# Kernel tuning notes

Measured on AMD Instinct MI355X. Metric: run time of the kernel, lower is better.

## Reference

```python
import jax, jax.numpy as jnp
import numpy as np

B, S, D, H = 2, 2048, 1024, 16
DK = D // H


def setup_inputs() -> dict:
    key = jax.random.key(0)
    ks = jax.random.split(key, 12)
    q = jax.random.normal(ks[0], (B, S, D), dtype=jnp.float32)
    k = jax.random.normal(ks[1], (B, S, D), dtype=jnp.float32)
    v = jax.random.normal(ks[2], (B, S, D), dtype=jnp.float32)
    # causal mask: 1 = attend, 0 = masked (masked_fill(mask==0, -inf))
    mask = jnp.tril(jnp.ones((S, S), dtype=jnp.int32))[None, None]
    w = 0.02
    Wq = jax.random.normal(ks[3], (D, D), dtype=jnp.float32) * w
    bq = jnp.zeros((D,), dtype=jnp.float32)
    Wk = jax.random.normal(ks[4], (D, D), dtype=jnp.float32) * w
    bk = jnp.zeros((D,), dtype=jnp.float32)
    Wv = jax.random.normal(ks[5], (D, D), dtype=jnp.float32) * w
    bv = jnp.zeros((D,), dtype=jnp.float32)
    Wo = jax.random.normal(ks[6], (D, D), dtype=jnp.float32) * w
    bo = jnp.zeros((D,), dtype=jnp.float32)
    return {"q": q, "k": k, "v": v, "mask": mask,
            "Wq": Wq, "bq": bq, "Wk": Wk, "bk": bk,
            "Wv": Wv, "bv": bv, "Wo": Wo, "bo": bo}


def _split_heads(x):
    b, s, _ = x.shape
    return x.reshape(b, s, H, DK).transpose(0, 2, 1, 3)  # [B,H,S,DK]


def reference(q, k, v, mask, Wq, bq, Wk, bk, Wv, bv, Wo, bo):
    qh = _split_heads(q @ Wq.T + bq)
    kh = _split_heads(k @ Wk.T + bk)
    vh = _split_heads(v @ Wv.T + bv)
    scale = 1.0 / jnp.sqrt(jnp.float32(DK))
    scores = jnp.einsum("bhqd,bhkd->bhqk", qh, kh) * scale  # [B,H,S,S]
    scores = jnp.where(mask == 0, -jnp.inf, scores)
    pesos = jax.nn.softmax(scores, axis=-1)
    pesos = jnp.nan_to_num(pesos, nan=0.0)  # fully-masked rows -> 0
    out = jnp.einsum("bhqk,bhkd->bhqd", pesos, vh)
    out = out.transpose(0, 2, 1, 3).reshape(q.shape[0], q.shape[1], D)
    # dropout is identity at inference
    return out @ Wo.T + bo
```

## Files before the change

### kernel.cpp

```cpp
#include <hip/hip_runtime.h>
#include <hip/hip_bf16.h>

#define B_  2
#define S_  2048
#define D_  1024
#define H_  16
#define DK_ 64

using bf16 = __hip_bfloat16;
typedef __bf16 bf16x8 __attribute__((ext_vector_type(8)));
typedef float  f32x4  __attribute__((ext_vector_type(4)));
typedef float  f32x16 __attribute__((ext_vector_type(16)));

__device__ inline void st1(float* p, float v) { *p = v; }
__device__ inline void st1(bf16*  p, float v) { *p = __float2bfloat16(v); }

__device__ inline void gll16(const bf16* g, bf16* l) {
    __builtin_amdgcn_global_load_lds(
        (const __attribute__((address_space(1))) unsigned int*)g,
        (__attribute__((address_space(3))) unsigned int*)l, 16, 0, 0);
}

__device__ inline f32x16 mfma32(bf16x8 a, bf16x8 b, f32x16 c) {
    return __builtin_amdgcn_mfma_f32_32x32x16_bf16(a, b, c, 0, 0, 0);
}

__device__ inline unsigned cvtpk(float lo, float hi) {
    unsigned r;
    asm("v_cvt_pk_bf16_f32 %0, %1, %2" : "=v"(r) : "v"(lo), "v"(hi));
    return r;
}

__device__ inline void plswap(unsigned &d, unsigned &s) {
    asm volatile("v_permlane32_swap_b32 %0, %1" : "+v"(d), "+v"(s));
}

__global__ __launch_bounds__(256) void cvt_kernel(
    const float* __restrict__ s0, const float* __restrict__ s1,
    const float* __restrict__ s2, const float* __restrict__ s3,
    const float* __restrict__ s4, const float* __restrict__ s5,
    const float* __restrict__ s6,
    bf16* __restrict__ d0, bf16* __restrict__ d1, bf16* __restrict__ d2,
    bf16* __restrict__ d3, bf16* __restrict__ d4, bf16* __restrict__ d5,
    bf16* __restrict__ d6, int nbig, int nsmall)
{
    const int z = blockIdx.y;
    const float* s; bf16* d; int n;
    switch (z) {
        case 0: s = s0; d = d0; n = nbig;   break;
        case 1: s = s1; d = d1; n = nbig;   break;
        case 2: s = s2; d = d2; n = nbig;   break;
        case 3: s = s3; d = d3; n = nsmall; break;
        case 4: s = s4; d = d4; n = nsmall; break;
        case 5: s = s5; d = d5; n = nsmall; break;
        default: s = s6; d = d6; n = nsmall; break;
    }
    const int idx = (blockIdx.x * 256 + threadIdx.x) * 4;
    if (idx < n) {
        const float4 v = *reinterpret_cast<const float4*>(s + idx);
        union { ushort4 u; __bf16 h[4]; } r;
        r.h[0] = (__bf16)v.x; r.h[1] = (__bf16)v.y;
        r.h[2] = (__bf16)v.z; r.h[3] = (__bf16)v.w;
        *reinterpret_cast<ushort4*>(d + idx) = r.u;
    }
}

template <typename TC, bool VT3, int BM>
__global__ __launch_bounds__(256, BM == 128 ? 3 : 4) void gemm_bt_kernel(
    const bf16* __restrict__ A0, const bf16* __restrict__ A1, const bf16* __restrict__ A2,
    const bf16* __restrict__ W0, const bf16* __restrict__ W1, const bf16* __restrict__ W2,
    const float* __restrict__ b0, const float* __restrict__ b1, const float* __restrict__ b2,
    TC* __restrict__ C0, TC* __restrict__ C1, TC* __restrict__ C2,
    int M, int N, int K)
{
    const int z = blockIdx.z;
    const bf16*  A    = (z == 0) ? A0 : (z == 1) ? A1 : A2;
    const bf16*  W    = (z == 0) ? W0 : (z == 1) ? W1 : W2;
    const float* bias = (z == 0) ? b0 : (z == 1) ? b1 : b2;
    TC*          C    = (z == 0) ? C0 : (z == 1) ? C1 : C2;

    __shared__ bf16 As[BM][32];
    __shared__ bf16 Bs[128][32];

    const int t    = threadIdx.x;
    const int lane = t & 63;
    const int wave = t >> 6;
    const int quad = lane >> 4;
    const int l16  = lane & 15;
    const int wm   = wave >> 1;
    const int wn   = wave & 1;

    const int m0 = blockIdx.y * BM;
    const int n0 = blockIdx.x * 128;

    constexpr int RPW = BM / 4;
    constexpr int MI  = BM / 32;
    const int ar0 = wave * RPW + (lane >> 2);
    const int br0 = wave * 32  + (lane >> 2);
    const int c0  = (lane & 3) * 8;
    const bf16* Ab = A + (size_t)(m0 + ar0) * K + c0;
    const bf16* Bb = W + (size_t)(n0 + br0) * K + c0;
    bf16* asd = &As[wave * RPW][0];
    bf16* bsd = &Bs[wave * 32][0];

    f32x4 acc[MI][4] = {};

    for (int kt = 0; kt < K; kt += 32) {
        __syncthreads();
        gll16(Ab + kt, asd);
        if constexpr (BM == 128) gll16(Ab + 16 * K + kt, asd + 16 * 32);
        gll16(Bb + kt, bsd);
        gll16(Bb + 16 * K + kt, bsd + 16 * 32);
        __syncthreads();

        bf16x8 af[MI], bfr[4];
#pragma unroll
        for (int mi = 0; mi < MI; mi++)
            af[mi] = *reinterpret_cast<const bf16x8*>(&As[wm * (BM / 2) + mi * 16 + l16][quad * 8]);
#pragma unroll
        for (int ni = 0; ni < 4; ni++)
            bfr[ni] = *reinterpret_cast<const bf16x8*>(&Bs[wn * 64 + ni * 16 + l16][quad * 8]);
#pragma unroll
        for (int mi = 0; mi < MI; mi++)
#pragma unroll
            for (int ni = 0; ni < 4; ni++)
                acc[mi][ni] = __builtin_amdgcn_mfma_f32_16x16x32_bf16(
                    af[mi], bfr[ni], acc[mi][ni], 0, 0, 0);
    }

    if (VT3 && z == 2) {
#pragma unroll
        for (int ni = 0; ni < 4; ni++) {
            const int col = n0 + wn * 64 + ni * 16 + l16;
            const float bvv = bias[col];
            const int hh = col >> 6, dh = col & 63;
#pragma unroll
            for (int mi = 0; mi < MI; mi++) {
                const int rb  = m0 + wm * (BM / 2) + mi * 16 + quad * 4;
                const int bb  = rb >> 11;
                const int tok = rb & (S_ - 1);
                union { ushort4 u; __bf16 h[4]; } pk;
#pragma unroll
                for (int i = 0; i < 4; i++)
                    pk.h[i] = (__bf16)(acc[mi][ni][i] + bvv);
                bf16* vt = (bf16*)C + ((size_t)(bb * H_ + hh) * DK_ + dh) * S_ + tok;
                *reinterpret_cast<ushort4*>(vt) = pk.u;
            }
        }
    } else {
#pragma unroll
        for (int ni = 0; ni < 4; ni++) {
            const int col = n0 + wn * 64 + ni * 16 + l16;
            const float bvv = bias[col];
#pragma unroll
            for (int mi = 0; mi < MI; mi++) {
#pragma unroll
                for (int i = 0; i < 4; i++) {
                    const int row = m0 + wm * (BM / 2) + mi * 16 + quad * 4 + i;
                    st1(&C[(size_t)row * N + col], acc[mi][ni][i] + bvv);
                }
            }
        }
    }
}

__global__ __launch_bounds__(256, 1) void attn_kernel(
    const bf16* __restrict__ Qp, const bf16* __restrict__ Kp,
    const bf16* __restrict__ VT, bf16* __restrict__ AO)
{
    const int t    = threadIdx.x;
    const int lane = t & 63;
    const int wave = t >> 6;
    const int r31  = lane & 31;
    const int hl   = lane >> 5;
    const int l7   = lane & 7;

    const int pairi = blockIdx.x;
    const int TL    = 15 - pairi;
    const int TS    = pairi;
    const int h = blockIdx.y;
    const int b = blockIdx.z;
    const size_t bh = (size_t)b * S_ * D_ + (size_t)h * DK_;
    const bf16* vtb = VT + (size_t)(b * H_ + h) * DK_ * S_;

    __shared__ bf16 Ks[4][64][64];
    __shared__ bf16 Vs[4][64][64];

    const int sR  = lane >> 3;
    const int scg = ((lane & 7) ^ sR) * 8;

    const float QSC = 0.18033688f;
    const float NEG = -1e30f;

    bf16x8 ONES;
#pragma unroll
    for (int j = 0; j < 8; j++) ONES[j] = (__bf16)1.0f;

    const int nA   = 2 * TL + 2;
    const int ntot = 34;

    int til = TL;
    bf16x8 qf[4];
    {
        const bf16* qr = Qp + bh + (size_t)(TL * 128 + wave * 32 + r31) * D_ + 8 * hl;
#pragma unroll
        for (int d = 0; d < 4; d++) {
            qf[d] = *reinterpret_cast<const bf16x8*>(qr + 16 * d);
#pragma unroll
            for (int j = 0; j < 8; j++) qf[d][j] = (__bf16)((float)qf[d][j] * QSC);
        }
    }

    f32x16 oacc0 = {}, oacc1 = {}, lacc = {};

    auto stage = [&](int slot) {
        const int k0n = ((slot < nA) ? slot : slot - nA) * 64;
        const int bb  = slot & 3;
#pragma unroll
        for (int j = 0; j < 2; j++) {
            const int rb = wave * 16 + j * 8;
            gll16(Kp + bh + (size_t)(k0n + rb + sR) * D_ + scg, &Ks[bb][rb][0]);
            gll16(vtb + (size_t)(rb + sR) * S_ + k0n + scg,     &Vs[bb][rb][0]);
        }
    };

    stage(0);
    stage(1);

    int kcbase = 0;
    for (int it = 0; it < ntot; it++) {
        if (it + 2 < ntot) {
            stage(it + 2);
            asm volatile("s_waitcnt vmcnt(8)" ::: "memory");
        } else if (it + 1 < ntot) {
            asm volatile("s_waitcnt vmcnt(4)" ::: "memory");
        } else {
            asm volatile("s_waitcnt vmcnt(0)" ::: "memory");
        }
        __builtin_amdgcn_s_barrier();

        if (it == nA) {
            const int qb0 = til * 128 + wave * 32;
#pragma unroll
            for (int r = 0; r < 16; r++) {
                const int q = qb0 + (r & 3) + 8 * (r >> 2) + 4 * hl;
                const float inv = 1.0f / lacc[r];
                AO[bh + (size_t)q * D_ + r31]      = __float2bfloat16(oacc0[r] * inv);
                AO[bh + (size_t)q * D_ + 32 + r31] = __float2bfloat16(oacc1[r] * inv);
            }
            til = TS; kcbase = nA;
            const bf16* qr = Qp + bh + (size_t)(TS * 128 + wave * 32 + r31) * D_ + 8 * hl;
#pragma unroll
            for (int d = 0; d < 4; d++) {
                qf[d] = *reinterpret_cast<const bf16x8*>(qr + 16 * d);
#pragma unroll
                for (int j = 0; j < 8; j++) qf[d][j] = (__bf16)((float)qf[d][j] * QSC);
            }
            oacc0 = f32x16{}; oacc1 = f32x16{}; lacc = f32x16{};
        }

        const int kc  = it - kcbase;
        const int k0  = kc * 64;
        const int buf = it & 3;
        const int qw0 = til * 128 + wave * 32;

        if (k0 <= qw0 + 31) {
            f32x16 s0 = {}, s1 = {};
#pragma unroll
            for (int d = 0; d < 4; d++) {
                const int g = ((2 * d + hl) ^ l7) * 8;
                const bf16x8 kf0 = *reinterpret_cast<const bf16x8*>(&Ks[buf][r31][g]);
                const bf16x8 kf1 = *reinterpret_cast<const bf16x8*>(&Ks[buf][32 + r31][g]);
                s0 = mfma32(kf0, qf[d], s0);
                s1 = mfma32(kf1, qf[d], s1);
            }

            if (k0 + 63 > qw0) {
                const int qg = qw0 + r31;
                const int kb = k0 + 4 * hl;
#pragma unroll
                for (int r = 0; r < 16; r++) {
                    const int ko = (r & 3) + 8 * (r >> 2);
                    s0[r] = (kb + ko      <= qg) ? s0[r] : NEG;
                    s1[r] = (kb + 32 + ko <= qg) ? s1[r] : NEG;
                }
            }

#pragma unroll
            for (int r = 0; r < 16; r++) {
                s0[r] = __builtin_amdgcn_exp2f(s0[r]);
                s1[r] = __builtin_amdgcn_exp2f(s1[r]);
            }

            bf16x8 pa[4];
#pragma unroll
            for (int G = 0; G < 2; G++) {
#pragma unroll
                for (int tt = 0; tt < 2; tt++) {
                    unsigned a01, a23, a45, a67;
                    if (G == 0) {
                        a01 = cvtpk(s0[8*tt+0], s0[8*tt+1]);
                        a23 = cvtpk(s0[8*tt+2], s0[8*tt+3]);
                        a45 = cvtpk(s0[8*tt+4], s0[8*tt+5]);
                        a67 = cvtpk(s0[8*tt+6], s0[8*tt+7]);
                    } else {
                        a01 = cvtpk(s1[8*tt+0], s1[8*tt+1]);
                        a23 = cvtpk(s1[8*tt+2], s1[8*tt+3]);
                        a45 = cvtpk(s1[8*tt+4], s1[8*tt+5]);
                        a67 = cvtpk(s1[8*tt+6], s1[8*tt+7]);
                    }
                    plswap(a01, a45);
                    plswap(a23, a67);
                    union { unsigned u[4]; bf16x8 v; } pu;
                    pu.u[0] = a01; pu.u[1] = a23; pu.u[2] = a45; pu.u[3] = a67;
                    pa[2 * G + tt] = pu.v;
                }
            }

#pragma unroll
            for (int s = 0; s < 4; s++) {
                const int g = ((2 * s + hl) ^ l7) * 8;
                const bf16x8 vf0 = *reinterpret_cast<const bf16x8*>(&Vs[buf][r31][g]);
                const bf16x8 vf1 = *reinterpret_cast<const bf16x8*>(&Vs[buf][32 + r31][g]);
                oacc0 = mfma32(pa[s], vf0, oacc0);
                oacc1 = mfma32(pa[s], vf1, oacc1);
                lacc  = mfma32(pa[s], ONES, lacc);
            }
        }
    }

    {
        const int qb0 = til * 128 + wave * 32;
#pragma unroll
        for (int r = 0; r < 16; r++) {
            const int q = qb0 + (r & 3) + 8 * (r >> 2) + 4 * hl;
            const float inv = 1.0f / lacc[r];
            AO[bh + (size_t)q * D_ + r31]      = __float2bfloat16(oacc0[r] * inv);
            AO[bh + (size_t)q * D_ + 32 + r31] = __float2bfloat16(oacc1[r] * inv);
        }
    }
}

extern "C" void kernel_launch(void* const* d_in, const int* in_sizes, int n_in,
                              void* d_out, int out_size, void* d_ws, size_t ws_size,
                              hipStream_t stream)
{
    const float* q  = (const float*)d_in[0];
    const float* k  = (const float*)d_in[1];
    const float* v  = (const float*)d_in[2];
    const float* Wq = (const float*)d_in[4];
    const float* bq = (const float*)d_in[5];
    const float* Wk = (const float*)d_in[6];
    const float* bk = (const float*)d_in[7];
    const float* Wv = (const float*)d_in[8];
    const float* bv = (const float*)d_in[9];
    const float* Wo = (const float*)d_in[10];
    const float* bo = (const float*)d_in[11];
    float* out = (float*)d_out;

    bf16* ws = (bf16*)d_ws;
    const size_t MD = (size_t)(B_ * S_) * D_;
    const size_t WN = (size_t)D_ * D_;
    bf16* qb  = ws;
    bf16* kb  = ws + MD;
    bf16* vb  = ws + 2 * MD;
    bf16* wqb = ws + 3 * MD;
    bf16* wkb = wqb + WN;
    bf16* wvb = wkb + WN;
    bf16* wob = wvb + WN;
    bf16* Qp  = wob + WN;
    bf16* Kp  = Qp + MD;
    bf16* VT  = Kp + MD;
    bf16* AO  = Qp;

    const int M = B_ * S_;

    cvt_kernel<<<dim3((int)(MD / 4 / 256), 7), 256, 0, stream>>>(
        q, k, v, Wq, Wk, Wv, Wo, qb, kb, vb, wqb, wkb, wvb, wob,
        (int)MD, (int)WN);

    gemm_bt_kernel<bf16, true, 128><<<dim3(D_ / 128, M / 128, 3), 256, 0, stream>>>(
        qb, kb, vb, wqb, wkb, wvb, bq, bk, bv, Qp, Kp, VT, M, D_, D_);

    attn_kernel<<<dim3(8, H_, B_), 256, 0, stream>>>(Qp, Kp, VT, AO);

    gemm_bt_kernel<float, false, 64><<<dim3(D_ / 128, M / 64, 1), 256, 0, stream>>>(
        AO, AO, AO, wob, wob, wob, bo, bo, bo, out, out, out, M, D_, D_);
}
```

Before: 241.8 us.

## Split paired causal tiles into separate blocks with heaviest-first scheduling

Each attention block used to process a pair of query tiles (long and short) so every block did the same work. Now every query tile gets its own block: 512 blocks on a 1D grid, with the heavy tiles ordered first, and launch bounds allow two blocks per CU. The goal is more parallelism and occupancy to hide latency on a GPU with many CUs, where 256 paired blocks may leave CUs idle. The cost is register pressure under the tighter launch bound, plus reliance on dispatch order for load balance.

Measured after the change: 225.2 us. -6.9%, faster.

```diff
diff --git a/kernel.cpp b/kernel.cpp
--- a/kernel.cpp
+++ b/kernel.cpp
@@ -164,7 +164,7 @@
     }
 }
 
-__global__ __launch_bounds__(256, 1) void attn_kernel(
+__global__ __launch_bounds__(256, 2) void attn_kernel(
     const bf16* __restrict__ Qp, const bf16* __restrict__ Kp,
     const bf16* __restrict__ VT, bf16* __restrict__ AO)
 {
@@ -175,11 +175,12 @@
     const int hl   = lane >> 5;
     const int l7   = lane & 7;
 
-    const int pairi = blockIdx.x;
-    const int TL    = 15 - pairi;
-    const int TS    = pairi;
-    const int h = blockIdx.y;
-    const int b = blockIdx.z;
+    const int bid = blockIdx.x;
+    int til, hb;
+    if (bid < 256) { til = 15 - (bid >> 5); hb = bid & 31; }
+    else           { til = (bid - 256) >> 5; hb = (bid - 256) & 31; }
+    const int h = hb & 15;
+    const int b = hb >> 4;
     const size_t bh = (size_t)b * S_ * D_ + (size_t)h * DK_;
     const bf16* vtb = VT + (size_t)(b * H_ + h) * DK_ * S_;
 
@@ -196,13 +197,11 @@
 #pragma unroll
     for (int j = 0; j < 8; j++) ONES[j] = (__bf16)1.0f;
 
-    const int nA   = 2 * TL + 2;
-    const int ntot = 34;
-
-    int til = TL;
+    const int ntot = 2 * til + 2;
+
     bf16x8 qf[4];
     {
-        const bf16* qr = Qp + bh + (size_t)(TL * 128 + wave * 32 + r31) * D_ + 8 * hl;
+        const bf16* qr = Qp + bh + (size_t)(til * 128 + wave * 32 + r31) * D_ + 8 * hl;
 #pragma unroll
         for (int d = 0; d < 4; d++) {
             qf[d] = *reinterpret_cast<const bf16x8*>(qr + 16 * d);
@@ -214,7 +213,7 @@
     f32x16 oacc0 = {}, oacc1 = {}, lacc = {};
 
     auto stage = [&](int slot) {
-        const int k0n = ((slot < nA) ? slot : slot - nA) * 64;
+        const int k0n = slot * 64;
         const int bb  = slot & 3;
 #pragma unroll
         for (int j = 0; j < 2; j++) {
@@ -227,7 +226,6 @@
     stage(0);
     stage(1);
 
-    int kcbase = 0;
     for (int it = 0; it < ntot; it++) {
         if (it + 2 < ntot) {
             stage(it + 2);
@@ -239,28 +237,7 @@
         }
         __builtin_amdgcn_s_barrier();
 
-        if (it == nA) {
-            const int qb0 = til * 128 + wave * 32;
-#pragma unroll
-            for (int r = 0; r < 16; r++) {
-                const int q = qb0 + (r & 3) + 8 * (r >> 2) + 4 * hl;
-                const float inv = 1.0f / lacc[r];
-                AO[bh + (size_t)q * D_ + r31]      = __float2bfloat16(oacc0[r] * inv);
-                AO[bh + (size_t)q * D_ + 32 + r31] = __float2bfloat16(oacc1[r] * inv);
-            }
-            til = TS; kcbase = nA;
-            const bf16* qr = Qp + bh + (size_t)(TS * 128 + wave * 32 + r31) * D_ + 8 * hl;
-#pragma unroll
-            for (int d = 0; d < 4; d++) {
-                qf[d] = *reinterpret_cast<const bf16x8*>(qr + 16 * d);
-#pragma unroll
-                for (int j = 0; j < 8; j++) qf[d][j] = (__bf16)((float)qf[d][j] * QSC);
-            }
-            oacc0 = f32x16{}; oacc1 = f32x16{}; lacc = f32x16{};
-        }
-
-        const int kc  = it - kcbase;
-        const int k0  = kc * 64;
+        const int k0  = it * 64;
         const int buf = it & 3;
         const int qw0 = til * 128 + wave * 32;
 
@@ -382,7 +359,7 @@
     gemm_bt_kernel<bf16, true, 128><<<dim3(D_ / 128, M / 128, 3), 256, 0, stream>>>(
         qb, kb, vb, wqb, wkb, wvb, bq, bk, bv, Qp, Kp, VT, M, D_, D_);
 
-    attn_kernel<<<dim3(8, H_, B_), 256, 0, stream>>>(Qp, Kp, VT, AO);
+    attn_kernel<<<dim3(512), 256, 0, stream>>>(Qp, Kp, VT, AO);
 
     gemm_bt_kernel<float, false, 64><<<dim3(D_ / 128, M / 64, 1), 256, 0, stream>>>(
         AO, AO, AO, wob, wob, wob, bo, bo, bo, out, out, out, M, D_, D_);
```
